# Optimization experiments

Hardware: AMD Instinct MI355X
Metric: run time of the kernel (lower is better)

## Reference

```python
import jax, jax.numpy as jnp
import numpy as np

B, N, DIM, H = 8, 2048, 64, 8  # per-head dim == DIM (module convention: inner_dim = dim * n_heads)


def setup_inputs() -> dict:
    key = jax.random.key(0)
    k1, k2, k3 = jax.random.split(key, 3)
    x = jax.random.normal(k1, (B, N, DIM), dtype=jnp.float32)
    W_qkv = jax.random.normal(k2, (DIM, 3 * H * DIM), dtype=jnp.float32) * (DIM ** -0.5)
    W_out = jax.random.normal(k3, (H * DIM, DIM), dtype=jnp.float32) * ((H * DIM) ** -0.5)
    b_out = jnp.zeros((DIM,), dtype=jnp.float32)
    return {"x": x, "W_qkv": W_qkv, "W_out": W_out, "b_out": b_out}


def reference(x, W_qkv, W_out, b_out):
    b, n, d = x.shape
    h = W_qkv.shape[1] // (3 * d)
    qkv = x @ W_qkv                                   # [b, n, 3*h*d]
    q, k, v = jnp.split(qkv, 3, axis=-1)              # each [b, n, h*d]
    def to_heads(t):
        return t.reshape(b, n, h, d).transpose(0, 2, 1, 3)  # [b, h, n, d]
    q, k, v = map(to_heads, (q, k, v))
    scale = d ** -0.5
    dot = jnp.einsum('bhid,bhjd->bhij', q, k) * scale  # [b, h, n, n]
    A = jax.nn.softmax(dot, axis=-1)
    z = jnp.einsum('bhij,bhjd->bhid', A, v)            # [b, h, n, d]
    z = z.transpose(0, 2, 1, 3).reshape(b, n, h * d)   # [b, n, h*d]
    return z @ W_out + b_out                           # [b, n, d]
```

## Files before the change

### kernel.cpp

```cpp
#include <hip/hip_runtime.h>
#include <math.h>

#define BB 8
#define NN 2048
#define DD 64
#define HH 8
#define BH (BB*HH)
#define HD (HH*DD)
#define NROWS (BB*NN)
#define QKV_COLS (3*HD)

typedef __bf16 bf16_8 __attribute__((ext_vector_type(8)));
typedef __bf16 bf16_4 __attribute__((ext_vector_type(4)));
typedef float  f32_16 __attribute__((ext_vector_type(16)));
typedef float  f32_4  __attribute__((ext_vector_type(4)));
typedef int    i32_2  __attribute__((ext_vector_type(2)));

#define QSCALE 0.180336880111f

__device__ __forceinline__ unsigned pack_bf16(float a, float b) {
  union { __bf16 h[2]; unsigned u; } t;
  t.h[0] = (__bf16)a; t.h[1] = (__bf16)b;
  return t.u;
}

__device__ __forceinline__ float fast_exp2(float x) {
#if __has_builtin(__builtin_amdgcn_exp2f)
  return __builtin_amdgcn_exp2f(x);
#else
  return __expf(x * 0.69314718056f);
#endif
}

__device__ __forceinline__ bf16_8 half_swap(unsigned a0, unsigned a1,
                                            unsigned a2, unsigned a3,
                                            int lhi, int xl) {
  union { unsigned u[4]; bf16_8 v; } F;
#if __has_builtin(__builtin_amdgcn_permlane32_swap)
  i32_2 r02 = __builtin_amdgcn_permlane32_swap((int)a0, (int)a2, false, false);
  i32_2 r13 = __builtin_amdgcn_permlane32_swap((int)a1, (int)a3, false, false);
  F.u[0] = (unsigned)r02.x; F.u[2] = (unsigned)r02.y;
  F.u[1] = (unsigned)r13.x; F.u[3] = (unsigned)r13.y;
#else
  unsigned w0 = (unsigned)__shfl((int)a0, xl, 64);
  unsigned w1 = (unsigned)__shfl((int)a1, xl, 64);
  unsigned w2 = (unsigned)__shfl((int)a2, xl, 64);
  unsigned w3 = (unsigned)__shfl((int)a3, xl, 64);
  F.u[0] = lhi ? w2 : a0;
  F.u[1] = lhi ? w3 : a1;
  F.u[2] = lhi ? a2 : w0;
  F.u[3] = lhi ? a3 : w1;
#endif
  return F.v;
}

__global__ __launch_bounds__(256) void qkv_kernel(
    const float* __restrict__ x, const float* __restrict__ Wqkv,
    const float* __restrict__ Wout,
    __bf16* __restrict__ Q, __bf16* __restrict__ K, __bf16* __restrict__ Vt,
    __bf16* __restrict__ Wob) {
  __shared__ __bf16 T[4][64][34];

  if (blockIdx.y == (NROWS / 128)) {
    int id = blockIdx.x * 256 + threadIdx.x;
    for (int e = id; e < 512 * 64; e += 24 * 256) {
      int kf = e >> 6, col = e & 63;
      int s = kf >> 4, lh = (kf >> 3) & 1, j = kf & 7;
      int t = col >> 5, lc = col & 31;
      Wob[((size_t)((t * 32 + s) * 64 + lh * 32 + lc)) * 8 + j] = (__bf16)Wout[e];
    }
    return;
  }

  const int lane = threadIdx.x & 63;
  const int wave = threadIdx.x >> 6;
  const int l31  = lane & 31, lhi = lane >> 5;
  const int cg   = blockIdx.x;
  const int row0 = blockIdx.y * 128 + wave * 32;

  const float* xr = x + (size_t)(row0 + l31) * 64 + lhi * 8;
  bf16_8 af[4];
#pragma unroll
  for (int s = 0; s < 4; s++) {
    f32_4 a0 = *(const f32_4*)(xr + s * 16);
    f32_4 a1 = *(const f32_4*)(xr + s * 16 + 4);
#pragma unroll
    for (int j = 0; j < 4; j++) { af[s][j] = (__bf16)a0[j]; af[s][4 + j] = (__bf16)a1[j]; }
  }

  const int col0  = cg * 64;
  const int which = col0 >> 9;
  const float wscl = (which == 0) ? QSCALE : 1.0f;

  f32_16 C0, C1;
#pragma unroll
  for (int i = 0; i < 16; i++) { C0[i] = 0.f; C1[i] = 0.f; }

#pragma unroll
  for (int s = 0; s < 4; s++) {
    bf16_8 b0, b1;
#pragma unroll
    for (int j = 0; j < 8; j++) {
      int k = s * 16 + lhi * 8 + j;
      b0[j] = (__bf16)(Wqkv[(size_t)k * QKV_COLS + col0 + l31]      * wscl);
      b1[j] = (__bf16)(Wqkv[(size_t)k * QKV_COLS + col0 + 32 + l31] * wscl);
    }
    C0 = __builtin_amdgcn_mfma_f32_32x32x16_bf16(af[s], b0, C0, 0, 0, 0);
    C1 = __builtin_amdgcn_mfma_f32_32x32x16_bf16(af[s], b1, C1, 0, 0, 0);
  }

  const int h   = (col0 >> 6) & 7;
  const int b   = row0 >> 11;
  const int n0l = row0 & 2047;

  if (which < 2) {
    __bf16* dst = (which == 0) ? Q : K;
#pragma unroll
    for (int r = 0; r < 16; r++) {
      int nl = (r & 3) + 8 * (r >> 2) + 4 * lhi;
      size_t base = (((size_t)(b * HH + h) * NN) + n0l + nl) * DD;
      dst[base + l31]      = (__bf16)C0[r];
      dst[base + 32 + l31] = (__bf16)C1[r];
    }
  } else {
    __bf16 (*Tw)[34] = T[wave];
#pragma unroll
    for (int r = 0; r < 16; r++) {
      int nl = (r & 3) + 8 * (r >> 2) + 4 * lhi;
      Tw[l31][nl]      = (__bf16)C0[r];
      Tw[32 + l31][nl] = (__bf16)C1[r];
    }
    __bf16* dst = Vt + (((size_t)(b * HH + h) * DD) + lane) * NN + n0l;
#pragma unroll
    for (int j = 0; j < 4; j++) {
      *(bf16_8*)(dst + j * 8) = *(const bf16_8*)(&Tw[lane][j * 8]);
    }
  }
}

#define TILE_ELEMS (128 * 72 + 64 * 136)
__global__ __launch_bounds__(512) void attn_kernel(
    const __bf16* __restrict__ Q, const __bf16* __restrict__ K,
    const __bf16* __restrict__ Vt, __bf16* __restrict__ z) {
  __shared__ __bf16 SMEM[2][TILE_ELEMS];

  const int tid  = threadIdx.x;
  const int wave = tid >> 6;
  const int lane = tid & 63;
  const int l31  = lane & 31;
  const int lhi  = lane >> 5;
  const int xl   = lane ^ 32;
  const int bh   = blockIdx.x >> 3;
  const int q0   = (blockIdx.x & 7) * 256 + wave * 32;

  const __bf16* Qbase = Q + ((size_t)bh * NN + q0 + l31) * DD + lhi * 8;
  bf16_8 qf[4];
#pragma unroll
  for (int s = 0; s < 4; s++) qf[s] = *(const bf16_8*)(Qbase + s * 16);

  f32_16 O0, O1;
#pragma unroll
  for (int i = 0; i < 16; i++) { O0[i] = 0.f; O1[i] = 0.f; }
  float ls0 = 0.f, ls1 = 0.f;

  const __bf16* Kb = K  + (size_t)bh * NN * DD;
  const __bf16* Vb = Vt + (size_t)bh * DD * NN;

  const int krow = tid >> 3, kcol = (tid & 7) * 8;
  const int vrow = tid >> 4, vcol = (tid & 15) * 8;
  const __bf16* kgl = Kb + (size_t)krow * 64 + kcol;
  const __bf16* vgl = Vb + (size_t)vrow * NN + vcol;
  const int koff0 = krow * 72 + kcol;
  const int voff0 = 128 * 72 + vrow * 136 + vcol;

  bf16_8 gk[2], gv[2];
#pragma unroll
  for (int i = 0; i < 2; i++) {
    gk[i] = *(const bf16_8*)(kgl + (size_t)i * 64 * 64);
    gv[i] = *(const bf16_8*)(vgl + (size_t)i * 32 * NN);
  }
  {
    __bf16* S = SMEM[0];
    *(bf16_8*)(S + koff0)            = gk[0];
    *(bf16_8*)(S + koff0 + 64 * 72)  = gk[1];
    *(bf16_8*)(S + voff0)            = gv[0];
    *(bf16_8*)(S + voff0 + 32 * 136) = gv[1];
  }
#pragma unroll
  for (int i = 0; i < 2; i++) {
    gk[i] = *(const bf16_8*)(kgl + (size_t)128 * 64 + (size_t)i * 64 * 64);
    gv[i] = *(const bf16_8*)(vgl + 128 + (size_t)i * 32 * NN);
  }
  __syncthreads();

  for (int it = 0; it < 16; it++) {
    __bf16* Ks = SMEM[it & 1];
    __bf16* Vs = SMEM[it & 1] + 128 * 72;

    if (it < 15) {
      __bf16* Sn = SMEM[(it + 1) & 1];
      *(bf16_8*)(Sn + koff0)            = gk[0];
      *(bf16_8*)(Sn + koff0 + 64 * 72)  = gk[1];
      *(bf16_8*)(Sn + voff0)            = gv[0];
      *(bf16_8*)(Sn + voff0 + 32 * 136) = gv[1];
      if (it < 14) {
        const size_t kadv = (size_t)(it + 2) * 128 * 64;
        const size_t vadv = (size_t)(it + 2) * 128;
#pragma unroll
        for (int i = 0; i < 2; i++) {
          gk[i] = *(const bf16_8*)(kgl + kadv + (size_t)i * 64 * 64);
          gv[i] = *(const bf16_8*)(vgl + vadv + (size_t)i * 32 * NN);
        }
      }
    }

#pragma unroll
    for (int hf = 0; hf < 2; hf++) {
      f32_16 S0, S1;
#pragma unroll
      for (int i = 0; i < 16; i++) { S0[i] = 0.f; S1[i] = 0.f; }
#pragma unroll
      for (int s = 0; s < 4; s++) {
        bf16_8 kb0 = *(const bf16_8*)(&Ks[(hf * 64 + l31) * 72 + s * 16 + lhi * 8]);
        bf16_8 kb1 = *(const bf16_8*)(&Ks[(hf * 64 + 32 + l31) * 72 + s * 16 + lhi * 8]);
        S0 = __builtin_amdgcn_mfma_f32_32x32x16_bf16(kb0, qf[s], S0, 0, 0, 0);
        S1 = __builtin_amdgcn_mfma_f32_32x32x16_bf16(kb1, qf[s], S1, 0, 0, 0);
      }

      unsigned pk[16];
#pragma unroll
      for (int t = 0; t < 8; t++) {
        float a = fast_exp2(S0[2 * t]), b = fast_exp2(S0[2 * t + 1]);
        float c = fast_exp2(S1[2 * t]), d = fast_exp2(S1[2 * t + 1]);
        ls0 += a + b;
        ls1 += c + d;
        pk[t]     = pack_bf16(a, b);
        pk[8 + t] = pack_bf16(c, d);
      }

#pragma unroll
      for (int g = 0; g < 4; g++) {
        const int base = (g >> 1) * 8 + (g & 1) * 4;
        bf16_8 F = half_swap(pk[base], pk[base + 1], pk[base + 2], pk[base + 3], lhi, xl);
        bf16_8 va0 = *(const bf16_8*)(&Vs[l31 * 136 + hf * 64 + g * 16 + lhi * 8]);
        bf16_8 va1 = *(const bf16_8*)(&Vs[(32 + l31) * 136 + hf * 64 + g * 16 + lhi * 8]);
        O0 = __builtin_amdgcn_mfma_f32_32x32x16_bf16(va0, F, O0, 0, 0, 0);
        O1 = __builtin_amdgcn_mfma_f32_32x32x16_bf16(va1, F, O1, 0, 0, 0);
      }
    }
    __syncthreads();
  }

  float lsum = ls0 + ls1;
  lsum += __shfl_xor(lsum, 32, 64);
  const float inv = 1.f / lsum;

  __bf16* ow = SMEM[0] + wave * (32 * 68);
#pragma unroll
  for (int g = 0; g < 4; g++) {
    bf16_4 p0, p1;
#pragma unroll
    for (int i = 0; i < 4; i++) {
      p0[i] = (__bf16)(O0[4 * g + i] * inv);
      p1[i] = (__bf16)(O1[4 * g + i] * inv);
    }
    const int d0 = 8 * g + 4 * lhi;
    *(bf16_4*)(ow + l31 * 68 + d0)      = p0;
    *(bf16_4*)(ow + l31 * 68 + 32 + d0) = p1;
  }
  const int b = bh >> 3, h = bh & 7;
  const int qr = lane >> 1, c0 = (lane & 1) * 32;
  __bf16* zp = z + ((size_t)b * NN + q0 + qr) * HD + h * DD + c0;
#pragma unroll
  for (int j = 0; j < 4; j++) {
    *(bf16_8*)(zp + 8 * j) = *(const bf16_8*)(ow + qr * 68 + c0 + 8 * j);
  }
}

__global__ __launch_bounds__(256) void out_proj_kernel(
    const __bf16* __restrict__ z, const __bf16* __restrict__ Wob,
    const float* __restrict__ bout, float* __restrict__ out) {
  __shared__ float red[3][64][33];
  const int tid  = threadIdx.x;
  const int wave = tid >> 6, lane = tid & 63;
  const int l31  = lane & 31, lhi = lane >> 5;
  const int row0 = blockIdx.x * 32;

  const __bf16* zr = z + (size_t)(row0 + l31) * HD + wave * 128 + lhi * 8;

  f32_16 C0, C1;
#pragma unroll
  for (int i = 0; i < 16; i++) { C0[i] = 0.f; C1[i] = 0.f; }

#pragma unroll
  for (int s = 0; s < 8; s++) {
    const int sa = wave * 8 + s;
    bf16_8 a  = *(const bf16_8*)(zr + s * 16);
    bf16_8 b0 = *(const bf16_8*)(Wob + ((size_t)((0 * 32 + sa) * 64 + lane)) * 8);
    bf16_8 b1 = *(const bf16_8*)(Wob + ((size_t)((1 * 32 + sa) * 64 + lane)) * 8);
    C0 = __builtin_amdgcn_mfma_f32_32x32x16_bf16(a, b0, C0, 0, 0, 0);
    C1 = __builtin_amdgcn_mfma_f32_32x32x16_bf16(a, b1, C1, 0, 0, 0);
  }

  if (wave) {
    float* rw = &red[wave - 1][lane][0];
#pragma unroll
    for (int r = 0; r < 16; r++) { rw[r] = C0[r]; rw[16 + r] = C1[r]; }
  }
  __syncthreads();
  if (wave == 0) {
    const float bi0 = bout[l31], bi1 = bout[32 + l31];
#pragma unroll
    for (int r = 0; r < 16; r++) {
      int n = row0 + (r & 3) + 8 * (r >> 2) + 4 * lhi;
      float v0 = C0[r] + red[0][lane][r]      + red[1][lane][r]      + red[2][lane][r];
      float v1 = C1[r] + red[0][lane][16 + r] + red[1][lane][16 + r] + red[2][lane][16 + r];
      out[(size_t)n * 64 + l31]      = v0 + bi0;
      out[(size_t)n * 64 + 32 + l31] = v1 + bi1;
    }
  }
}

extern "C" void kernel_launch(void* const* d_in, const int* in_sizes, int n_in,
                              void* d_out, int out_size, void* d_ws, size_t ws_size,
                              hipStream_t stream) {
  const float* x    = (const float*)d_in[0];
  const float* Wqkv = (const float*)d_in[1];
  const float* Wout = (const float*)d_in[2];
  const float* bout = (const float*)d_in[3];
  float* out = (float*)d_out;

  const size_t buf_elems = (size_t)BB * HH * NN * DD;
  __bf16* Qw  = (__bf16*)d_ws;
  __bf16* Kw  = Qw  + buf_elems;
  __bf16* Vtw = Kw  + buf_elems;
  __bf16* zw  = Vtw + buf_elems;
  __bf16* Wob = zw  + buf_elems;

  qkv_kernel<<<dim3(QKV_COLS / 64, NROWS / 128 + 1), 256, 0, stream>>>(
      x, Wqkv, Wout, Qw, Kw, Vtw, Wob);
  attn_kernel<<<BH * (NN / 256), 512, 0, stream>>>(Qw, Kw, Vtw, zw);
  out_proj_kernel<<<NROWS / 32, 256, 0, stream>>>(zw, Wob, bout, out);
}
```

Before: 181.9 us.

## Process 64 query rows per wave to reuse K/V tiles across two subtiles

Each wave now handles two 32-row query subtiles (64 rows), so each K/V fragment read from shared memory feeds twice as many MFMAs, and each block covers 512 queries. The grid is halved, so the K/V global loads and LDS staging are amortized over more work. The cost is doubled accumulator and score registers per wave, which may lower occupancy or cause spills. Only 256 blocks are launched, which may underfill the GPU's compute units.

Result: no change. 180.0 us (-1.0%).

```diff
diff --git a/kernel.cpp b/kernel.cpp
--- a/kernel.cpp
+++ b/kernel.cpp
@@ -150,18 +150,21 @@
   const int l31  = lane & 31;
   const int lhi  = lane >> 5;
   const int xl   = lane ^ 32;
-  const int bh   = blockIdx.x >> 3;
-  const int q0   = (blockIdx.x & 7) * 256 + wave * 32;
+  const int bh   = blockIdx.x >> 2;
+  const int q0   = (blockIdx.x & 3) * 512 + wave * 64;
 
   const __bf16* Qbase = Q + ((size_t)bh * NN + q0 + l31) * DD + lhi * 8;
-  bf16_8 qf[4];
-#pragma unroll
-  for (int s = 0; s < 4; s++) qf[s] = *(const bf16_8*)(Qbase + s * 16);
-
-  f32_16 O0, O1;
-#pragma unroll
-  for (int i = 0; i < 16; i++) { O0[i] = 0.f; O1[i] = 0.f; }
-  float ls0 = 0.f, ls1 = 0.f;
+  bf16_8 qfa[4], qfb[4];
+#pragma unroll
+  for (int s = 0; s < 4; s++) {
+    qfa[s] = *(const bf16_8*)(Qbase + s * 16);
+    qfb[s] = *(const bf16_8*)(Qbase + (size_t)32 * DD + s * 16);
+  }
+
+  f32_16 O0a, O1a, O0b, O1b;
+#pragma unroll
+  for (int i = 0; i < 16; i++) { O0a[i] = 0.f; O1a[i] = 0.f; O0b[i] = 0.f; O1b[i] = 0.f; }
+  float lsa = 0.f, lsb = 0.f;
 
   const __bf16* Kb = K  + (size_t)bh * NN * DD;
   const __bf16* Vb = Vt + (size_t)bh * DD * NN;
@@ -216,64 +219,80 @@
 
 #pragma unroll
     for (int hf = 0; hf < 2; hf++) {
-      f32_16 S0, S1;
-#pragma unroll
-      for (int i = 0; i < 16; i++) { S0[i] = 0.f; S1[i] = 0.f; }
+      f32_16 S0a, S1a, S0b, S1b;
+#pragma unroll
+      for (int i = 0; i < 16; i++) { S0a[i] = 0.f; S1a[i] = 0.f; S0b[i] = 0.f; S1b[i] = 0.f; }
 #pragma unroll
       for (int s = 0; s < 4; s++) {
         bf16_8 kb0 = *(const bf16_8*)(&Ks[(hf * 64 + l31) * 72 + s * 16 + lhi * 8]);
         bf16_8 kb1 = *(const bf16_8*)(&Ks[(hf * 64 + 32 + l31) * 72 + s * 16 + lhi * 8]);
-        S0 = __builtin_amdgcn_mfma_f32_32x32x16_bf16(kb0, qf[s], S0, 0, 0, 0);
-        S1 = __builtin_amdgcn_mfma_f32_32x32x16_bf16(kb1, qf[s], S1, 0, 0, 0);
-      }
-
-      unsigned pk[16];
+        S0a = __builtin_amdgcn_mfma_f32_32x32x16_bf16(kb0, qfa[s], S0a, 0, 0, 0);
+        S1a = __builtin_amdgcn_mfma_f32_32x32x16_bf16(kb1, qfa[s], S1a, 0, 0, 0);
+        S0b = __builtin_amdgcn_mfma_f32_32x32x16_bf16(kb0, qfb[s], S0b, 0, 0, 0);
+        S1b = __builtin_amdgcn_mfma_f32_32x32x16_bf16(kb1, qfb[s], S1b, 0, 0, 0);
+      }
+
+      unsigned pka[16], pkb[16];
 #pragma unroll
       for (int t = 0; t < 8; t++) {
-        float a = fast_exp2(S0[2 * t]), b = fast_exp2(S0[2 * t + 1]);
-        float c = fast_exp2(S1[2 * t]), d = fast_exp2(S1[2 * t + 1]);
-        ls0 += a + b;
-        ls1 += c + d;
-        pk[t]     = pack_bf16(a, b);
-        pk[8 + t] = pack_bf16(c, d);
+        float a0 = fast_exp2(S0a[2 * t]), a1 = fast_exp2(S0a[2 * t + 1]);
+        float a2 = fast_exp2(S1a[2 * t]), a3 = fast_exp2(S1a[2 * t + 1]);
+        lsa += (a0 + a1) + (a2 + a3);
+        pka[t]     = pack_bf16(a0, a1);
+        pka[8 + t] = pack_bf16(a2, a3);
+        float b0 = fast_exp2(S0b[2 * t]), b1 = fast_exp2(S0b[2 * t + 1]);
+        float b2 = fast_exp2(S1b[2 * t]), b3 = fast_exp2(S1b[2 * t + 1]);
+        lsb += (b0 + b1) + (b2 + b3);
+        pkb[t]     = pack_bf16(b0, b1);
+        pkb[8 + t] = pack_bf16(b2, b3);
       }
 
 #pragma unroll
       for (int g = 0; g < 4; g++) {
         const int base = (g >> 1) * 8 + (g & 1) * 4;
-        bf16_8 F = half_swap(pk[base], pk[base + 1], pk[base + 2], pk[base + 3], lhi, xl);
         bf16_8 va0 = *(const bf16_8*)(&Vs[l31 * 136 + hf * 64 + g * 16 + lhi * 8]);
         bf16_8 va1 = *(const bf16_8*)(&Vs[(32 + l31) * 136 + hf * 64 + g * 16 + lhi * 8]);
-        O0 = __builtin_amdgcn_mfma_f32_32x32x16_bf16(va0, F, O0, 0, 0, 0);
-        O1 = __builtin_amdgcn_mfma_f32_32x32x16_bf16(va1, F, O1, 0, 0, 0);
+        bf16_8 Fa = half_swap(pka[base], pka[base + 1], pka[base + 2], pka[base + 3], lhi, xl);
+        O0a = __builtin_amdgcn_mfma_f32_32x32x16_bf16(va0, Fa, O0a, 0, 0, 0);
+        O1a = __builtin_amdgcn_mfma_f32_32x32x16_bf16(va1, Fa, O1a, 0, 0, 0);
+        bf16_8 Fb = half_swap(pkb[base], pkb[base + 1], pkb[base + 2], pkb[base + 3], lhi, xl);
+        O0b = __builtin_amdgcn_mfma_f32_32x32x16_bf16(va0, Fb, O0b, 0, 0, 0);
+        O1b = __builtin_amdgcn_mfma_f32_32x32x16_bf16(va1, Fb, O1b, 0, 0, 0);
       }
     }
     __syncthreads();
   }
 
-  float lsum = ls0 + ls1;
-  lsum += __shfl_xor(lsum, 32, 64);
-  const float inv = 1.f / lsum;
-
+  lsa += __shfl_xor(lsa, 32, 64);
+  lsb += __shfl_xor(lsb, 32, 64);
+  const float inva = 1.f / lsa;
+  const float invb = 1.f / lsb;
+
+  const int b = bh >> 3, h = bh & 7;
   __bf16* ow = SMEM[0] + wave * (32 * 68);
-#pragma unroll
-  for (int g = 0; g < 4; g++) {
-    bf16_4 p0, p1;
-#pragma unroll
-    for (int i = 0; i < 4; i++) {
-      p0[i] = (__bf16)(O0[4 * g + i] * inv);
-      p1[i] = (__bf16)(O1[4 * g + i] * inv);
-    }
-    const int d0 = 8 * g + 4 * lhi;
-    *(bf16_4*)(ow + l31 * 68 + d0)      = p0;
-    *(bf16_4*)(ow + l31 * 68 + 32 + d0) = p1;
-  }
-  const int b = bh >> 3, h = bh & 7;
   const int qr = lane >> 1, c0 = (lane & 1) * 32;
-  __bf16* zp = z + ((size_t)b * NN + q0 + qr) * HD + h * DD + c0;
-#pragma unroll
-  for (int j = 0; j < 4; j++) {
-    *(bf16_8*)(zp + 8 * j) = *(const bf16_8*)(ow + qr * 68 + c0 + 8 * j);
+#pragma unroll
+  for (int sub = 0; sub < 2; sub++) {
+    const f32_16& P0 = sub ? O0b : O0a;
+    const f32_16& P1 = sub ? O1b : O1a;
+    const float inv = sub ? invb : inva;
+#pragma unroll
+    for (int g = 0; g < 4; g++) {
+      bf16_4 p0, p1;
+#pragma unroll
+      for (int i = 0; i < 4; i++) {
+        p0[i] = (__bf16)(P0[4 * g + i] * inv);
+        p1[i] = (__bf16)(P1[4 * g + i] * inv);
+      }
+      const int d0 = 8 * g + 4 * lhi;
+      *(bf16_4*)(ow + l31 * 68 + d0)      = p0;
+      *(bf16_4*)(ow + l31 * 68 + 32 + d0) = p1;
+    }
+    __bf16* zp = z + ((size_t)b * NN + q0 + sub * 32 + qr) * HD + h * DD + c0;
+#pragma unroll
+    for (int j = 0; j < 4; j++) {
+      *(bf16_8*)(zp + 8 * j) = *(const bf16_8*)(ow + qr * 68 + c0 + 8 * j);
+    }
   }
 }
 
@@ -339,6 +358,6 @@
 
   qkv_kernel<<<dim3(QKV_COLS / 64, NROWS / 128 + 1), 256, 0, stream>>>(
       x, Wqkv, Wout, Qw, Kw, Vtw, Wob);
-  attn_kernel<<<BH * (NN / 256), 512, 0, stream>>>(Qw, Kw, Vtw, zw);
+  attn_kernel<<<BH * (NN / 512), 512, 0, stream>>>(Qw, Kw, Vtw, zw);
   out_proj_kernel<<<NROWS / 32, 256, 0, stream>>>(zw, Wob, bout, out);
 }
```
